# Performance work log

Hardware: AMD Instinct MI355X
Metric: run time of the kernel (lower is better)

Reference implementation:

```python
import jax, jax.numpy as jnp
import numpy as np

H = 8  # num_heads
C = 512  # embed_dims
L = 3  # num_layers
SCALE = (C // H) ** -0.5


def _ln(x, g, b, eps=1e-5):
    mu = jnp.mean(x, axis=-1, keepdims=True)
    var = jnp.mean((x - mu) ** 2, axis=-1, keepdims=True)
    return g * (x - mu) / jnp.sqrt(var + eps) + b


def setup_inputs() -> dict:
    key = jax.random.key(0)
    ks = jax.random.split(key, 12)
    B, Nq, Nk = 16, 64, 4096
    s = 0.02
    return dict(
        queries=jax.random.normal(ks[0], (B, Nq, C), jnp.float32),
        feat=jax.random.normal(ks[1], (B, Nk, C), jnp.float32),
        extra_token=jax.random.normal(ks[2], (B, 1, C), jnp.float32),
        Wq=jax.random.normal(ks[3], (L, C, C), jnp.float32) * s,
        bq=jnp.zeros((L, C), jnp.float32),
        Wk=jax.random.normal(ks[4], (L, C, C), jnp.float32) * s,
        bk=jnp.zeros((L, C), jnp.float32),
        Wv=jax.random.normal(ks[5], (L, C, C), jnp.float32) * s,
        bv=jnp.zeros((L, C), jnp.float32),
        Wo=jax.random.normal(ks[6], (L, C, C), jnp.float32) * s,
        bo=jnp.zeros((L, C), jnp.float32),
        W1=jax.random.normal(ks[7], (L, C, 4 * C), jnp.float32) * s,
        b1=jnp.zeros((L, 4 * C), jnp.float32),
        W2=jax.random.normal(ks[8], (L, 4 * C, C), jnp.float32) * s,
        b2=jnp.zeros((L, C), jnp.float32),
        g2=jnp.ones((L, C), jnp.float32),
        beta2=jnp.zeros((L, C), jnp.float32),
        g3=jnp.ones((L, C), jnp.float32),
        beta3=jnp.zeros((L, C), jnp.float32),
    )


def reference(queries, feat, extra_token, Wq, bq, Wk, bk, Wv, bv, Wo, bo,
              W1, b1, W2, b2, g2, beta2, g3, beta3):
    B, Nq, _ = queries.shape
    Nk = feat.shape[1]
    hd = C // H
    # extra gating token is NOT projected through q: raw reshape -> [B,H,1,hd]
    eq = extra_token.reshape(B, 1, H, hd).transpose(0, 2, 1, 3)
    x = queries
    outs, attns, affs = [], [], []
    for i in range(L):
        q = (x @ Wq[i] + bq[i]).reshape(B, Nq, H, hd).transpose(0, 2, 1, 3)
        k = (feat @ Wk[i] + bk[i]).reshape(B, Nk, H, hd).transpose(0, 2, 1, 3)
        v = (feat @ Wv[i] + bv[i]).reshape(B, Nk, H, hd).transpose(0, 2, 1, 3)
        attn = jnp.einsum('bhqd,bhkd->bhqk', q, k) * SCALE  # pre-softmax scores
        # affinity gate from extra token, averaged over heads -> [B,1,1,Nk]
        aff = jax.nn.sigmoid(jnp.mean(
            jnp.einsum('bhod,bhkd->bhok', eq, k) * SCALE, axis=1, keepdims=True))
        p = aff * jax.nn.softmax(attn, axis=-1)  # gated probabilities
        o = jnp.einsum('bhqk,bhkd->bqhd', p, v).reshape(B, Nq, C)
        o = o @ Wo[i] + bo[i]
        x = _ln(x + o, g2[i], beta2[i])
        ff = jax.nn.relu(x @ W1[i] + b1[i]) @ W2[i] + b2[i]
        x = _ln(x + ff, g3[i], beta3[i])
        outs.append(x)
        attns.append(attn.sum(axis=1) / H)  # head-averaged pre-softmax scores
        affs.append(aff)
    return (jnp.stack(outs), jnp.stack(attns), jnp.stack(affs))
```

## Files before the change

### kernel.cpp

```cpp
#include <hip/hip_runtime.h>


typedef unsigned short u16;
typedef __attribute__((ext_vector_type(8))) short short8;
typedef __attribute__((ext_vector_type(4))) short short4v;
typedef __attribute__((ext_vector_type(4))) float f32x4;

__device__ __forceinline__ float b2f(u16 u) {
    union { unsigned int i; float f; } v; v.i = ((unsigned int)u) << 16; return v.f;
}
__device__ __forceinline__ u16 f2b(float f) {
    unsigned int x = __float_as_uint(f);
    x += 0x7fffu + ((x >> 16) & 1u);
    return (u16)(x >> 16);
}

__device__ __forceinline__ float waveSum(float v) {
#pragma unroll
    for (int o = 32; o > 0; o >>= 1) v += __shfl_xor(v, o);
    return v;
}

__device__ __forceinline__ void gl_lds16(const void* g, void* l) {
    __builtin_amdgcn_global_load_lds(
        (__attribute__((address_space(1))) void*)g,
        (__attribute__((address_space(3))) void*)l, 16, 0, 0);
}

__global__ __launch_bounds__(256) void fattn_k(
    const u16* __restrict__ q16, const u16* __restrict__ K16,
    const u16* __restrict__ VT16, float* __restrict__ Op,
    float2* __restrict__ ml)
{
    __shared__ u16 Qs[64][64];
    __shared__ u16 Ks[128][64];
    __shared__ u16 Vs[64][128];
    __shared__ u16 Ps[64][128];
    const int t = threadIdx.x;
    const int lane = t & 63;
    const int w = t >> 6;
    const int bh = blockIdx.y;
    const int split = blockIdx.x;
    const int b = bh >> 3, h = bh & 7;
    const int kbase = split * 1024;
    const int rl = lane & 15, uq = lane >> 4;
    const int r0 = (lane >> 4) * 4;
    const int c0 = lane & 15;
    const int srow8 = lane >> 3, up8 = lane & 7;
    const int srow4 = lane >> 4, up16 = lane & 15;

#pragma unroll
    for (int rnd = 0; rnd < 2; ++rnd) {
        const int row = rnd * 32 + w * 8 + srow8;
        const int ul = up8 ^ (row & 7);
        gl_lds16(q16 + ((long)(b * 64 + row)) * 512 + h * 64 + ul * 8,
                 &Qs[rnd * 32 + w * 8][0]);
    }

    f32x4 O[4];
#pragma unroll
    for (int n = 0; n < 4; ++n) O[n] = (f32x4){0.f, 0.f, 0.f, 0.f};
    float m_run[4] = {-3.0e38f, -3.0e38f, -3.0e38f, -3.0e38f};
    float l_run[4] = {0.f, 0.f, 0.f, 0.f};

    const int R = w * 16 + rl;

    for (int tt = 0; tt < 8; ++tt) {
        __syncthreads();
#pragma unroll
        for (int rnd = 0; rnd < 4; ++rnd) {
            const int row = rnd * 32 + w * 8 + srow8;
            const int ul = up8 ^ (row & 7);
            gl_lds16(K16 + ((long)(b * 4096 + kbase + tt * 128 + row)) * 512
                         + h * 64 + ul * 8,
                     &Ks[rnd * 32 + w * 8][0]);
        }
#pragma unroll
        for (int rnd = 0; rnd < 4; ++rnd) {
            const int row = rnd * 16 + w * 4 + srow4;
            const int ul = up16 ^ (row & 15);
            gl_lds16(VT16 + (long)b * 2097152 + ((long)(h * 64 + row)) * 4096
                         + kbase + tt * 128 + ul * 8,
                     &Vs[rnd * 16 + w * 4][0]);
        }
        __syncthreads();

        f32x4 s[8];
        short8 af[2];
#pragma unroll
        for (int kc = 0; kc < 2; ++kc)
            af[kc] = *(const short8*)(&Qs[R][((kc * 4 + uq) ^ (R & 7)) * 8]);
#pragma unroll
        for (int j = 0; j < 8; ++j) {
            s[j] = (f32x4){0.f, 0.f, 0.f, 0.f};
            const int Rb = j * 16 + rl;
#pragma unroll
            for (int kc = 0; kc < 2; ++kc) {
                short8 bf = *(const short8*)(&Ks[Rb][((kc * 4 + uq) ^ (Rb & 7)) * 8]);
                s[j] = __builtin_amdgcn_mfma_f32_16x16x32_bf16(af[kc], bf, s[j], 0, 0, 0);
            }
        }
#pragma unroll
        for (int j = 0; j < 8; ++j)
#pragma unroll
            for (int r = 0; r < 4; ++r) s[j][r] *= 0.125f;

        float mv[4];
#pragma unroll
        for (int r = 0; r < 4; ++r) {
            float m = s[0][r];
#pragma unroll
            for (int j = 1; j < 8; ++j) m = fmaxf(m, s[j][r]);
#pragma unroll
            for (int mask = 1; mask < 16; mask <<= 1)
                m = fmaxf(m, __shfl_xor(m, mask));
            mv[r] = m;
        }
        float al[4], rs[4];
#pragma unroll
        for (int r = 0; r < 4; ++r) {
            const float mn = fmaxf(m_run[r], mv[r]);
            al[r] = __expf(m_run[r] - mn);
            m_run[r] = mn;
            rs[r] = 0.f;
        }
#pragma unroll
        for (int j = 0; j < 8; ++j)
#pragma unroll
            for (int r = 0; r < 4; ++r) {
                s[j][r] = __expf(s[j][r] - m_run[r]);
                rs[r] += s[j][r];
            }
#pragma unroll
        for (int r = 0; r < 4; ++r) {
#pragma unroll
            for (int mask = 1; mask < 16; mask <<= 1)
                rs[r] += __shfl_xor(rs[r], mask);
            l_run[r] = l_run[r] * al[r] + rs[r];
        }
#pragma unroll
        for (int n = 0; n < 4; ++n)
#pragma unroll
            for (int r = 0; r < 4; ++r) O[n][r] *= al[r];

#pragma unroll
        for (int j = 0; j < 8; ++j)
#pragma unroll
            for (int r = 0; r < 4; ++r) {
                const int row = w * 16 + r0 + r;
                const int col = j * 16 + c0;
                Ps[row][(((col >> 3) ^ (row & 15)) << 3) + (col & 7)] = f2b(s[j][r]);
            }
#pragma unroll
        for (int kc4 = 0; kc4 < 4; ++kc4) {
            const short8 afp = *(const short8*)(&Ps[R][(((kc4 * 4 + uq) ^ (R & 15)) << 3)]);
#pragma unroll
            for (int n = 0; n < 4; ++n) {
                const int Rv = n * 16 + rl;
                const short8 bfv = *(const short8*)(&Vs[Rv][(((kc4 * 4 + uq) ^ (Rv & 15)) << 3)]);
                O[n] = __builtin_amdgcn_mfma_f32_16x16x32_bf16(afp, bfv, O[n], 0, 0, 0);
            }
        }
    }

    const long obase = ((long)(split * 128 + bh)) * 64;
#pragma unroll
    for (int n = 0; n < 4; ++n)
#pragma unroll
        for (int r = 0; r < 4; ++r) {
            const int q = w * 16 + r0 + r;
            Op[(obase + q) * 64 + n * 16 + c0] = O[n][r];
        }
    if (c0 == 0) {
#pragma unroll
        for (int r = 0; r < 4; ++r) {
            const int q = w * 16 + r0 + r;
            ml[obase + q] = make_float2(m_run[r], l_run[r]);
        }
    }
}

__global__ __launch_bounds__(256) void fmerge_k(
    const float* __restrict__ Op, const float2* __restrict__ ml,
    u16* __restrict__ o16)
{
    const int i = blockIdx.x * 256 + threadIdx.x;
    const int d4 = i & 15;
    const int q  = (i >> 4) & 63;
    const int bh = i >> 10;
    const float2 m0 = ml[((long)(0 * 128 + bh)) * 64 + q];
    const float2 m1 = ml[((long)(1 * 128 + bh)) * 64 + q];
    const float2 m2 = ml[((long)(2 * 128 + bh)) * 64 + q];
    const float2 m3 = ml[((long)(3 * 128 + bh)) * 64 + q];
    const float m = fmaxf(fmaxf(m0.x, m1.x), fmaxf(m2.x, m3.x));
    const float e0 = __expf(m0.x - m), e1 = __expf(m1.x - m);
    const float e2 = __expf(m2.x - m), e3 = __expf(m3.x - m);
    const float inv = 1.f / (m0.y * e0 + m1.y * e1 + m2.y * e2 + m3.y * e3);
    const float4 v0 = *(const float4*)(Op + (((long)(0 * 128 + bh)) * 64 + q) * 64 + d4 * 4);
    const float4 v1 = *(const float4*)(Op + (((long)(1 * 128 + bh)) * 64 + q) * 64 + d4 * 4);
    const float4 v2 = *(const float4*)(Op + (((long)(2 * 128 + bh)) * 64 + q) * 64 + d4 * 4);
    const float4 v3 = *(const float4*)(Op + (((long)(3 * 128 + bh)) * 64 + q) * 64 + d4 * 4);
    float4 acc;
    acc.x = (v0.x * e0 + v1.x * e1 + v2.x * e2 + v3.x * e3) * inv;
    acc.y = (v0.y * e0 + v1.y * e1 + v2.y * e2 + v3.y * e3) * inv;
    acc.z = (v0.z * e0 + v1.z * e1 + v2.z * e2 + v3.z * e3) * inv;
    acc.w = (v0.w * e0 + v1.w * e1 + v2.w * e2 + v3.w * e3) * inv;
    const int b = bh >> 3, h = bh & 7;
    short4v r;
    r[0] = (short)f2b(acc.x); r[1] = (short)f2b(acc.y);
    r[2] = (short)f2b(acc.z); r[3] = (short)f2b(acc.w);
    *(short4v*)(o16 + (long)b * 32768 + q * 512 + h * 64 + d4 * 4) = r;
}

template<bool BIAS_ROW, bool HAS_BIAS, bool AFFC>
__global__ __launch_bounds__(512, 1) void gemm256x256_k(
    const u16* __restrict__ A, const u16* __restrict__ Bt,
    const float* __restrict__ bias, u16* __restrict__ Cout,
    int lda, int ldb, int ldc, long sA2, long sB2, long sC2,
    const float* __restrict__ affc)
{
    __shared__ u16 As[2][256][64];
    __shared__ u16 Bs[2][256][64];
    const int t = threadIdx.x;
    const int lane = t & 63;
    const int wave = t >> 6;

    const int gx = gridDim.x, gy = gridDim.y;
    const int nwg = gx * gy * gridDim.z;
    int id;
    {
        const int orig = blockIdx.x + blockIdx.y * gx + blockIdx.z * gx * gy;
        const int qq = nwg >> 3, rr = nwg & 7;
        const int xcd = orig & 7, sub = orig >> 3;
        id = (xcd < rr ? xcd * (qq + 1) : rr * (qq + 1) + (xcd - rr) * qq) + sub;
    }
    const int bx = id % gx;
    const int by = (id / gx) % gy;
    const int z  = id / (gx * gy);

    A  += (long)z * sA2;
    Bt += (long)z * sB2;
    const long cbase = (long)z * sC2;
    const int n0 = bx * 256;
    const int m0 = by * 256;
    const int wm = wave >> 2;
    const int wn = wave & 3;
    const int rl = lane & 15, uq = lane >> 4;
    const int srow = lane >> 3;
    const int up   = lane & 7;

    f32x4 acc[8][4];
#pragma unroll
    for (int i = 0; i < 8; ++i)
#pragma unroll
        for (int j = 0; j < 4; ++j) acc[i][j] = (f32x4){0.f, 0.f, 0.f, 0.f};

    auto stage = [&](int buf, int kt) {
        const int k0 = kt * 64;
#pragma unroll
        for (int r = 0; r < 4; ++r) {
            const int row = r * 64 + wave * 8 + srow;
            const int ul = up ^ (row & 7);
            gl_lds16(A + (long)(m0 + row) * lda + k0 + ul * 8,
                     &As[buf][r * 64 + wave * 8][0]);
        }
#pragma unroll
        for (int r = 0; r < 4; ++r) {
            const int row = r * 64 + wave * 8 + srow;
            const int ul = up ^ (row & 7);
            gl_lds16(Bt + (long)(n0 + row) * ldb + k0 + ul * 8,
                     &Bs[buf][r * 64 + wave * 8][0]);
        }
    };

    auto compute = [&](int buf) {
#pragma unroll
        for (int kc = 0; kc < 2; ++kc) {
            short8 af[8], bf[4];
#pragma unroll
            for (int i = 0; i < 8; ++i) {
                const int R = wm * 128 + i * 16 + rl;
                af[i] = *(const short8*)(&As[buf][R][((kc * 4 + uq) ^ (R & 7)) * 8]);
            }
#pragma unroll
            for (int j = 0; j < 4; ++j) {
                const int R = wn * 64 + j * 16 + rl;
                bf[j] = *(const short8*)(&Bs[buf][R][((kc * 4 + uq) ^ (R & 7)) * 8]);
            }
            __builtin_amdgcn_s_setprio(1);
#pragma unroll
            for (int i = 0; i < 8; ++i)
#pragma unroll
                for (int j = 0; j < 4; ++j)
                    acc[i][j] = __builtin_amdgcn_mfma_f32_16x16x32_bf16(
                        af[i], bf[j], acc[i][j], 0, 0, 0);
            __builtin_amdgcn_s_setprio(0);
        }
    };

    stage(0, 0);
    __syncthreads();
    int buf = 0;
#pragma unroll
    for (int kt = 0; kt < 8; ++kt) {
        if (kt + 1 < 8) stage(buf ^ 1, kt + 1);
        compute(buf);
        __syncthreads();
        buf ^= 1;
    }

    const int r0 = (lane >> 4) * 4;
    const int c0 = lane & 15;
#pragma unroll
    for (int i = 0; i < 8; ++i) {
#pragma unroll
        for (int j = 0; j < 4; ++j) {
#pragma unroll
            for (int r = 0; r < 4; ++r) {
                const int row = m0 + wm * 128 + i * 16 + r0 + r;
                const int col = n0 + wn * 64 + j * 16 + c0;
                float v = acc[i][j][r];
                if constexpr (HAS_BIAS) {
                    if constexpr (BIAS_ROW) v += bias[row]; else v += bias[col];
                }
                if constexpr (AFFC) v *= affc[(long)z * 4096 + col];
                Cout[cbase + (long)row * ldc + col] = f2b(v);
            }
        }
    }
}

template<int TM, int TN, bool OUT_BF16, bool RELU, bool BIAS_ROW, bool HAS_BIAS>
__global__ __launch_bounds__(256) void gemm_bt_k(
    const u16* __restrict__ A, const u16* __restrict__ Bt,
    const float* __restrict__ bias, void* __restrict__ Cout,
    int K, int lda, int ldb, int ldc,
    long sA1, long sB1, long sC1, float alpha)
{
    __shared__ u16 As[TM][64];
    __shared__ u16 Bs[TN][64];
    const int t = threadIdx.x;
    const int lane = t & 63;
    const int wave = t >> 6;
    const int z = blockIdx.z;
    A  += (long)z * sA1;
    Bt += (long)z * sB1;
    const long cbase = (long)z * sC1;
    const int n0 = blockIdx.x * TN;
    const int m0 = blockIdx.y * TM;
    constexpr int FM = TM / 32, FN = TN / 32;
    const int wr = wave >> 1, wc = wave & 1;
    const int rl = lane & 15, uq = lane >> 4;

    f32x4 acc[FM][FN];
#pragma unroll
    for (int i = 0; i < FM; ++i)
#pragma unroll
        for (int j = 0; j < FN; ++j) acc[i][j] = (f32x4){0.f, 0.f, 0.f, 0.f};

    const int srow = lane >> 3;
    const int up   = lane & 7;

    for (int k0 = 0; k0 < K; k0 += 64) {
        __syncthreads();
#pragma unroll
        for (int r = 0; r < TM / 32; ++r) {
            const int br = (wave * (TM / 32) + r) * 8;
            const int row = br + srow;
            const int ul = up ^ (row & 7);
            gl_lds16(A + (long)(m0 + row) * lda + k0 + ul * 8, &As[br][0]);
        }
#pragma unroll
        for (int r = 0; r < TN / 32; ++r) {
            const int br = (wave * (TN / 32) + r) * 8;
            const int row = br + srow;
            const int ul = up ^ (row & 7);
            gl_lds16(Bt + (long)(n0 + row) * ldb + k0 + ul * 8, &Bs[br][0]);
        }
        __syncthreads();

#pragma unroll
        for (int kc = 0; kc < 2; ++kc) {
            short8 af[FM], bf[FN];
#pragma unroll
            for (int i = 0; i < FM; ++i) {
                const int R = wr * (TM / 2) + i * 16 + rl;
                af[i] = *(const short8*)(&As[R][((kc * 4 + uq) ^ (R & 7)) * 8]);
            }
#pragma unroll
            for (int j = 0; j < FN; ++j) {
                const int R = wc * (TN / 2) + j * 16 + rl;
                bf[j] = *(const short8*)(&Bs[R][((kc * 4 + uq) ^ (R & 7)) * 8]);
            }
#pragma unroll
            for (int i = 0; i < FM; ++i)
#pragma unroll
                for (int j = 0; j < FN; ++j)
                    acc[i][j] = __builtin_amdgcn_mfma_f32_16x16x32_bf16(
                        af[i], bf[j], acc[i][j], 0, 0, 0);
        }
    }

    const int r0 = (lane >> 4) * 4;
    const int c0 = lane & 15;
#pragma unroll
    for (int i = 0; i < FM; ++i) {
#pragma unroll
        for (int j = 0; j < FN; ++j) {
#pragma unroll
            for (int r = 0; r < 4; ++r) {
                const int row = m0 + wr * (TM / 2) + i * 16 + r0 + r;
                const int col = n0 + wc * (TN / 2) + j * 16 + c0;
                float v = acc[i][j][r] * alpha;
                if constexpr (HAS_BIAS) {
                    if constexpr (BIAS_ROW) v += bias[row]; else v += bias[col];
                }
                if constexpr (RELU) v = fmaxf(v, 0.f);
                const long idx = cbase + (long)row * ldc + col;
                if constexpr (OUT_BF16) ((u16*)Cout)[idx] = f2b(v);
                else                    ((float*)Cout)[idx] = v;
            }
        }
    }
}

__global__ __launch_bounds__(256) void ffred_k(
    const float* __restrict__ part, const float* __restrict__ bias,
    float* __restrict__ out)
{
    const int i = (blockIdx.x * 256 + threadIdx.x) * 4;
    const int c = i & 511;
    float4 s = *(const float4*)(part + i);
#pragma unroll
    for (int sp = 1; sp < 4; ++sp) {
        const float4 v = *(const float4*)(part + (long)sp * 524288 + i);
        s.x += v.x; s.y += v.y; s.z += v.z; s.w += v.w;
    }
    s.x += bias[c]; s.y += bias[c + 1]; s.z += bias[c + 2]; s.w += bias[c + 3];
    *(float4*)(out + i) = s;
}

__global__ __launch_bounds__(256) void umat_k(
    const float* __restrict__ Wk, const float* __restrict__ extra,
    float* __restrict__ u)
{
    __shared__ float ex[16][512];
    const int l = blockIdx.x;
    const int t = threadIdx.x;
    for (int i = t; i < 16 * 512 / 4; i += 256)
        ((float4*)&ex[0][0])[i] = ((const float4*)extra)[i];
    __syncthreads();
    const int lane = t & 63, wave = t >> 6;
    const int row = blockIdx.y * 4 + wave;
    const float* wrow = Wk + ((size_t)l * 512 + row) * 512 + lane * 8;
    float w[8];
#pragma unroll
    for (int j = 0; j < 8; ++j) w[j] = wrow[j];
    float s[16];
#pragma unroll
    for (int b = 0; b < 16; ++b) {
        float x = 0.f;
#pragma unroll
        for (int j = 0; j < 8; ++j) x += w[j] * ex[b][lane * 8 + j];
        s[b] = waveSum(x);
    }
    if (lane < 16) u[((size_t)l * 16 + lane) * 512 + row] = s[lane];
}

__global__ __launch_bounds__(256) void cbk_k(
    const float* __restrict__ bk, const float* __restrict__ extra,
    float* __restrict__ cb)
{
    const int gw = blockIdx.x * 4 + (threadIdx.x >> 6);
    const int lane = threadIdx.x & 63;
    const int l = gw >> 4, b = gw & 15;
    float s = 0.f;
#pragma unroll
    for (int j = 0; j < 8; ++j)
        s += extra[b * 512 + lane * 8 + j] * bk[l * 512 + lane * 8 + j];
    s = waveSum(s);
    if (lane == 0) cb[gw] = s;
}

__global__ __launch_bounds__(256) void cvt16_aff_k(
    const float* __restrict__ feat, u16* __restrict__ dst,
    const float* __restrict__ u, const float* __restrict__ cb,
    float* __restrict__ affb, float* __restrict__ affs_out)
{
    const int t = blockIdx.x * 256 + threadIdx.x;
    const long i = (long)t * 8;
    const int lane = threadIdx.x & 63;
    const int r = t >> 6;
    const int b = r >> 12;
    const float4 a0 = *(const float4*)(feat + i);
    const float4 a1 = *(const float4*)(feat + i + 4);
    short8 o;
    o[0] = (short)f2b(a0.x); o[1] = (short)f2b(a0.y);
    o[2] = (short)f2b(a0.z); o[3] = (short)f2b(a0.w);
    o[4] = (short)f2b(a1.x); o[5] = (short)f2b(a1.y);
    o[6] = (short)f2b(a1.z); o[7] = (short)f2b(a1.w);
    *(short8*)(dst + i) = o;
    const float f[8] = {a0.x, a0.y, a0.z, a0.w, a1.x, a1.y, a1.z, a1.w};
#pragma unroll
    for (int l = 0; l < 3; ++l) {
        const float* ur = u + ((size_t)l * 16 + b) * 512 + lane * 8;
        float s = 0.f;
#pragma unroll
        for (int j = 0; j < 8; ++j) s += f[j] * ur[j];
        s = waveSum(s);
        if (lane == 0) {
            const float av = 1.f / (1.f + __expf(-0.015625f * (s + cb[l * 16 + b])));
            affb[l * 65536 + r] = av;
            affs_out[l * 65536 + r] = av;
        }
    }
}

template<bool WRITE_OUT>
__global__ __launch_bounds__(256) void ln_k(
    float* __restrict__ x, const float* __restrict__ add,
    const float* __restrict__ g, const float* __restrict__ be,
    u16* __restrict__ x16, float* __restrict__ outp)
{
    const int r = blockIdx.x, t = threadIdx.x;
    const int w = t >> 6, lane = t & 63;
    __shared__ float red[4];
    float* xr = x + (long)r * 512;
    const float* ar = add + (long)r * 512;
    const float v0 = xr[2 * t]     + ar[2 * t];
    const float v1 = xr[2 * t + 1] + ar[2 * t + 1];
    float s = waveSum(v0 + v1);
    if (lane == 0) red[w] = s;
    __syncthreads();
    s = red[0] + red[1] + red[2] + red[3];
    const float mu = s * (1.f / 512.f);
    const float d0 = v0 - mu, d1 = v1 - mu;
    __syncthreads();
    float vs = waveSum(d0 * d0 + d1 * d1);
    if (lane == 0) red[w] = vs;
    __syncthreads();
    vs = red[0] + red[1] + red[2] + red[3];
    const float rs = rsqrtf(vs * (1.f / 512.f) + 1e-5f);
    const float o0 = g[2 * t]     * d0 * rs + be[2 * t];
    const float o1 = g[2 * t + 1] * d1 * rs + be[2 * t + 1];
    xr[2 * t] = o0; xr[2 * t + 1] = o1;
    x16[(long)r * 512 + 2 * t]     = f2b(o0);
    x16[(long)r * 512 + 2 * t + 1] = f2b(o1);
    if constexpr (WRITE_OUT) {
        outp[(long)r * 512 + 2 * t]     = o0;
        outp[(long)r * 512 + 2 * t + 1] = o1;
    }
}

__global__ __launch_bounds__(256) void initx_k(
    const float* __restrict__ src, float* __restrict__ x, u16* __restrict__ x16)
{
    const long i = ((long)blockIdx.x * 256 + threadIdx.x) * 8;
    const float4 a = *(const float4*)(src + i);
    const float4 b = *(const float4*)(src + i + 4);
    *(float4*)(x + i) = a;
    *(float4*)(x + i + 4) = b;
    short8 r;
    r[0] = (short)f2b(a.x); r[1] = (short)f2b(a.y); r[2] = (short)f2b(a.z); r[3] = (short)f2b(a.w);
    r[4] = (short)f2b(b.x); r[5] = (short)f2b(b.y); r[6] = (short)f2b(b.z); r[7] = (short)f2b(b.w);
    *(short8*)(x16 + i) = r;
}

__global__ __launch_bounds__(256) void transpose_w_k(
    const float* __restrict__ W, u16* __restrict__ WT, int K, int N)
{
    __shared__ float tile[32][33];
    const int z = blockIdx.z;
    W  += (size_t)z * K * N;
    WT += (size_t)z * K * N;
    const int n0 = blockIdx.x * 32, k0 = blockIdx.y * 32;
    const int tx = threadIdx.x & 31, ty = threadIdx.x >> 5;
#pragma unroll
    for (int j = 0; j < 32; j += 8)
        tile[ty + j][tx] = W[(size_t)(k0 + ty + j) * N + n0 + tx];
    __syncthreads();
#pragma unroll
    for (int j = 0; j < 32; j += 8)
        WT[(size_t)(n0 + ty + j) * K + k0 + tx] = f2b(tile[tx][ty + j]);
}

extern "C" void kernel_launch(void* const* d_in, const int* in_sizes, int n_in,
                              void* d_out, int out_size, void* d_ws, size_t ws_size,
                              hipStream_t stream)
{
    (void)in_sizes; (void)n_in; (void)out_size; (void)ws_size;
    const float* queries = (const float*)d_in[0];
    const float* feat    = (const float*)d_in[1];
    const float* extra   = (const float*)d_in[2];
    const float* Wq = (const float*)d_in[3];  const float* bq = (const float*)d_in[4];
    const float* Wk = (const float*)d_in[5];  const float* bk = (const float*)d_in[6];
    const float* Wv = (const float*)d_in[7];  const float* bv = (const float*)d_in[8];
    const float* Wo = (const float*)d_in[9];  const float* bo = (const float*)d_in[10];
    const float* W1 = (const float*)d_in[11]; const float* b1 = (const float*)d_in[12];
    const float* W2 = (const float*)d_in[13]; const float* b2 = (const float*)d_in[14];
    const float* g2 = (const float*)d_in[15]; const float* be2 = (const float*)d_in[16];
    const float* g3 = (const float*)d_in[17]; const float* be3 = (const float*)d_in[18];

    char* wsb = (char*)d_ws;
    size_t off = 0;
    auto alloc = [&](size_t bytes) -> char* {
        char* p = wsb + off; off += (bytes + 255) & ~(size_t)255; return p;
    };
    u16*  feat16 = (u16*)alloc(33554432ull * 2);
    u16*  WqT = (u16*)alloc(786432ull * 2);
    u16*  WkT = (u16*)alloc(786432ull * 2);
    u16*  WvT = (u16*)alloc(786432ull * 2);
    u16*  WoT = (u16*)alloc(786432ull * 2);
    u16*  W1T = (u16*)alloc(3145728ull * 2);
    u16*  W2T = (u16*)alloc(3145728ull * 2);
    u16*  K16 = (u16*)alloc(33554432ull * 2);
    u16*  VT16 = (u16*)alloc(33554432ull * 2);
    u16*  q16 = (u16*)alloc(524288ull * 2);
    float* Op  = (float*)alloc(4194304ull * 4);
    float2* ml = (float2*)alloc(32768ull * 8);
    float* affb  = (float*)alloc(196608ull * 4);
    u16*  o16 = (u16*)alloc(524288ull * 2);
    float* oproj = (float*)alloc(524288ull * 4);
    float* xb    = (float*)alloc(524288ull * 4);
    u16*  x16 = (u16*)alloc(524288ull * 2);
    u16*  h116 = (u16*)alloc(2097152ull * 2);
    float* ffb   = (float*)alloc(524288ull * 4);
    float* uvec  = (float*)alloc(24576ull * 4);
    float* cb    = (float*)alloc(48ull * 4);
    float* part2 = (float*)VT16;

    float* out_f = (float*)d_out;
    float* outs_base  = out_f;
    float* attns_base = out_f + 1572864;
    float* affs_base  = out_f + 14155776;

    umat_k<<<dim3(3, 128), 256, 0, stream>>>(Wk, extra, uvec);
    cbk_k<<<12, 256, 0, stream>>>(bk, extra, cb);
    cvt16_aff_k<<<16384, 256, 0, stream>>>(feat, feat16, uvec, cb, affb, affs_base);
    initx_k<<<256, 256, 0, stream>>>(queries, xb, x16);
    transpose_w_k<<<dim3(16, 16, 3), 256, 0, stream>>>(Wq, WqT, 512, 512);
    transpose_w_k<<<dim3(16, 16, 3), 256, 0, stream>>>(Wk, WkT, 512, 512);
    transpose_w_k<<<dim3(16, 16, 3), 256, 0, stream>>>(Wv, WvT, 512, 512);
    transpose_w_k<<<dim3(16, 16, 3), 256, 0, stream>>>(Wo, WoT, 512, 512);
    transpose_w_k<<<dim3(64, 16, 3), 256, 0, stream>>>(W1, W1T, 512, 2048);
    transpose_w_k<<<dim3(16, 64, 3), 256, 0, stream>>>(W2, W2T, 2048, 512);

    for (int i = 0; i < 3; ++i) {
        gemm256x256_k<false, true, false><<<dim3(2, 256, 1), 512, 0, stream>>>(
            feat16, WkT + i * 262144, bk + i * 512, K16,
            512, 512, 512, 0, 0, 0, nullptr);
        gemm256x256_k<true, true, true><<<dim3(16, 2, 16), 512, 0, stream>>>(
            WvT + i * 262144, feat16, bv + i * 512, VT16,
            512, 512, 4096, 0, 2097152, 2097152, affb + i * 65536);
        gemm_bt_k<64, 64, true, false, false, true>
            <<<dim3(8, 16, 1), 256, 0, stream>>>(
            x16, WqT + i * 262144, bq + i * 512, q16,
            512, 512, 512, 512, 0, 0, 0, 1.f);
        gemm_bt_k<64, 128, false, false, false, false>
            <<<dim3(32, 1, 16), 256, 0, stream>>>(
            q16, K16, nullptr, attns_base + (size_t)i * 4194304,
            512, 512, 512, 4096, 32768, 2097152, 262144, 0.015625f);
        fattn_k<<<dim3(4, 128), 256, 0, stream>>>(q16, K16, VT16, Op, ml);
        fmerge_k<<<512, 256, 0, stream>>>(Op, ml, o16);
        gemm_bt_k<64, 64, false, false, false, true>
            <<<dim3(8, 16, 1), 256, 0, stream>>>(
            o16, WoT + i * 262144, bo + i * 512, oproj,
            512, 512, 512, 512, 0, 0, 0, 1.f);
        ln_k<false><<<1024, 256, 0, stream>>>(xb, oproj, g2 + i * 512, be2 + i * 512, x16, nullptr);
        gemm_bt_k<64, 128, true, true, false, true>
            <<<dim3(16, 16, 1), 256, 0, stream>>>(
            x16, W1T + (size_t)i * 1048576, b1 + i * 2048, h116,
            512, 512, 512, 2048, 0, 0, 0, 1.f);
        gemm_bt_k<64, 64, false, false, false, false>
            <<<dim3(8, 16, 4), 256, 0, stream>>>(
            h116, W2T + (size_t)i * 1048576, nullptr, part2,
            512, 2048, 2048, 512, 512, 512, 524288, 1.f);
        ffred_k<<<512, 256, 0, stream>>>(part2, b2 + i * 512, ffb);
        ln_k<true><<<1024, 256, 0, stream>>>(xb, ffb, g3 + i * 512, be3 + i * 512, x16,
                                             outs_base + (size_t)i * 524288);
    }
}
```

Measured before the change: 670.1 us.

## Interleave global-to-LDS staging with MFMA phases in 256x256 GEMM

Result: slower. 688.7 us (+2.8%).

```diff
diff --git a/kernel.cpp b/kernel.cpp
--- a/kernel.cpp
+++ b/kernel.cpp
@@ -25,6 +25,136 @@
     __builtin_amdgcn_global_load_lds(
         (__attribute__((address_space(1))) void*)g,
         (__attribute__((address_space(3))) void*)l, 16, 0, 0);
+}
+
+template<bool BIAS_ROW, bool HAS_BIAS, bool AFFC>
+__global__ __launch_bounds__(512, 1) void gemm256x256_k(
+    const u16* __restrict__ A, const u16* __restrict__ Bt,
+    const float* __restrict__ bias, u16* __restrict__ Cout,
+    int lda, int ldb, int ldc, long sA2, long sB2, long sC2,
+    const float* __restrict__ affc)
+{
+    __shared__ u16 As[2][256][64];
+    __shared__ u16 Bs[2][256][64];
+    const int t = threadIdx.x;
+    const int lane = t & 63;
+    const int wave = t >> 6;
+
+    const int gx = gridDim.x, gy = gridDim.y;
+    const int nwg = gx * gy * gridDim.z;
+    int id;
+    {
+        const int orig = blockIdx.x + blockIdx.y * gx + blockIdx.z * gx * gy;
+        const int qq = nwg >> 3, rr = nwg & 7;
+        const int xcd = orig & 7, sub = orig >> 3;
+        id = (xcd < rr ? xcd * (qq + 1) : rr * (qq + 1) + (xcd - rr) * qq) + sub;
+    }
+    const int bx = id % gx;
+    const int by = (id / gx) % gy;
+    const int z  = id / (gx * gy);
+
+    A  += (long)z * sA2;
+    Bt += (long)z * sB2;
+    const long cbase = (long)z * sC2;
+    const int n0 = bx * 256;
+    const int m0 = by * 256;
+    const int wm = wave >> 2;
+    const int wn = wave & 3;
+    const int rl = lane & 15, uq = lane >> 4;
+    const int srow = lane >> 3;
+    const int up   = lane & 7;
+
+    f32x4 acc[8][4];
+#pragma unroll
+    for (int i = 0; i < 8; ++i)
+#pragma unroll
+        for (int j = 0; j < 4; ++j) acc[i][j] = (f32x4){0.f, 0.f, 0.f, 0.f};
+
+    auto stage_round = [&](int buf, int kt, int rnd) {
+        const int k0 = kt * 64;
+        if (rnd < 4) {
+            const int row = rnd * 64 + wave * 8 + srow;
+            const int ul = up ^ (row & 7);
+            gl_lds16(A + (long)(m0 + row) * lda + k0 + ul * 8,
+                     &As[buf][rnd * 64 + wave * 8][0]);
+        } else {
+            const int r = rnd - 4;
+            const int row = r * 64 + wave * 8 + srow;
+            const int ul = up ^ (row & 7);
+            gl_lds16(Bt + (long)(n0 + row) * ldb + k0 + ul * 8,
+                     &Bs[buf][r * 64 + wave * 8][0]);
+        }
+    };
+
+#pragma unroll
+    for (int rnd = 0; rnd < 8; ++rnd) stage_round(0, 0, rnd);
+    __syncthreads();
+
+    int buf = 0;
+    for (int kt = 0; kt < 8; ++kt) {
+        const int nbuf = buf ^ 1;
+        short8 bf[2][4];
+#pragma unroll
+        for (int p = 0; p < 4; ++p) {
+            if (kt < 7) {
+                stage_round(nbuf, kt + 1, p * 2);
+                stage_round(nbuf, kt + 1, p * 2 + 1);
+            }
+            if (p == 0) {
+#pragma unroll
+                for (int kc = 0; kc < 2; ++kc)
+#pragma unroll
+                    for (int j = 0; j < 4; ++j) {
+                        const int Rb = wn * 64 + j * 16 + rl;
+                        bf[kc][j] = *(const short8*)(
+                            &Bs[buf][Rb][((kc * 4 + uq) ^ (Rb & 7)) * 8]);
+                    }
+            }
+            short8 af[2][2];
+#pragma unroll
+            for (int kc = 0; kc < 2; ++kc)
+#pragma unroll
+                for (int i2 = 0; i2 < 2; ++i2) {
+                    const int Ra = wm * 128 + (p * 2 + i2) * 16 + rl;
+                    af[kc][i2] = *(const short8*)(
+                        &As[buf][Ra][((kc * 4 + uq) ^ (Ra & 7)) * 8]);
+                }
+            __builtin_amdgcn_s_barrier();
+            __builtin_amdgcn_s_setprio(1);
+#pragma unroll
+            for (int kc = 0; kc < 2; ++kc)
+#pragma unroll
+                for (int i2 = 0; i2 < 2; ++i2)
+#pragma unroll
+                    for (int j = 0; j < 4; ++j)
+                        acc[p * 2 + i2][j] = __builtin_amdgcn_mfma_f32_16x16x32_bf16(
+                            af[kc][i2], bf[kc][j], acc[p * 2 + i2][j], 0, 0, 0);
+            __builtin_amdgcn_s_setprio(0);
+            if (p < 3) __builtin_amdgcn_s_barrier();
+        }
+        __syncthreads();
+        buf = nbuf;
+    }
+
+    const int r0 = (lane >> 4) * 4;
+    const int c0 = lane & 15;
+#pragma unroll
+    for (int i = 0; i < 8; ++i) {
+#pragma unroll
+        for (int j = 0; j < 4; ++j) {
+#pragma unroll
+            for (int r = 0; r < 4; ++r) {
+                const int row = m0 + wm * 128 + i * 16 + r0 + r;
+                const int col = n0 + wn * 64 + j * 16 + c0;
+                float v = acc[i][j][r];
+                if constexpr (HAS_BIAS) {
+                    if constexpr (BIAS_ROW) v += bias[row]; else v += bias[col];
+                }
+                if constexpr (AFFC) v *= affc[(long)z * 4096 + col];
+                Cout[cbase + (long)row * ldc + col] = f2b(v);
+            }
+        }
+    }
 }
 
 __global__ __launch_bounds__(256) void fattn_k(
@@ -210,124 +340,6 @@
     r[0] = (short)f2b(acc.x); r[1] = (short)f2b(acc.y);
     r[2] = (short)f2b(acc.z); r[3] = (short)f2b(acc.w);
     *(short4v*)(o16 + (long)b * 32768 + q * 512 + h * 64 + d4 * 4) = r;
-}
-
-template<bool BIAS_ROW, bool HAS_BIAS, bool AFFC>
-__global__ __launch_bounds__(512, 1) void gemm256x256_k(
-    const u16* __restrict__ A, const u16* __restrict__ Bt,
-    const float* __restrict__ bias, u16* __restrict__ Cout,
-    int lda, int ldb, int ldc, long sA2, long sB2, long sC2,
-    const float* __restrict__ affc)
-{
-    __shared__ u16 As[2][256][64];
-    __shared__ u16 Bs[2][256][64];
-    const int t = threadIdx.x;
-    const int lane = t & 63;
-    const int wave = t >> 6;
-
-    const int gx = gridDim.x, gy = gridDim.y;
-    const int nwg = gx * gy * gridDim.z;
-    int id;
-    {
-        const int orig = blockIdx.x + blockIdx.y * gx + blockIdx.z * gx * gy;
-        const int qq = nwg >> 3, rr = nwg & 7;
-        const int xcd = orig & 7, sub = orig >> 3;
-        id = (xcd < rr ? xcd * (qq + 1) : rr * (qq + 1) + (xcd - rr) * qq) + sub;
-    }
-    const int bx = id % gx;
-    const int by = (id / gx) % gy;
-    const int z  = id / (gx * gy);
-
-    A  += (long)z * sA2;
-    Bt += (long)z * sB2;
-    const long cbase = (long)z * sC2;
-    const int n0 = bx * 256;
-    const int m0 = by * 256;
-    const int wm = wave >> 2;
-    const int wn = wave & 3;
-    const int rl = lane & 15, uq = lane >> 4;
-    const int srow = lane >> 3;
-    const int up   = lane & 7;
-
-    f32x4 acc[8][4];
-#pragma unroll
-    for (int i = 0; i < 8; ++i)
-#pragma unroll
-        for (int j = 0; j < 4; ++j) acc[i][j] = (f32x4){0.f, 0.f, 0.f, 0.f};
-
-    auto stage = [&](int buf, int kt) {
-        const int k0 = kt * 64;
-#pragma unroll
-        for (int r = 0; r < 4; ++r) {
-            const int row = r * 64 + wave * 8 + srow;
-            const int ul = up ^ (row & 7);
-            gl_lds16(A + (long)(m0 + row) * lda + k0 + ul * 8,
-                     &As[buf][r * 64 + wave * 8][0]);
-        }
-#pragma unroll
-        for (int r = 0; r < 4; ++r) {
-            const int row = r * 64 + wave * 8 + srow;
-            const int ul = up ^ (row & 7);
-            gl_lds16(Bt + (long)(n0 + row) * ldb + k0 + ul * 8,
-                     &Bs[buf][r * 64 + wave * 8][0]);
-        }
-    };
-
-    auto compute = [&](int buf) {
-#pragma unroll
-        for (int kc = 0; kc < 2; ++kc) {
-            short8 af[8], bf[4];
-#pragma unroll
-            for (int i = 0; i < 8; ++i) {
-                const int R = wm * 128 + i * 16 + rl;
-                af[i] = *(const short8*)(&As[buf][R][((kc * 4 + uq) ^ (R & 7)) * 8]);
-            }
-#pragma unroll
-            for (int j = 0; j < 4; ++j) {
-                const int R = wn * 64 + j * 16 + rl;
-                bf[j] = *(const short8*)(&Bs[buf][R][((kc * 4 + uq) ^ (R & 7)) * 8]);
-            }
-            __builtin_amdgcn_s_setprio(1);
-#pragma unroll
-            for (int i = 0; i < 8; ++i)
-#pragma unroll
-                for (int j = 0; j < 4; ++j)
-                    acc[i][j] = __builtin_amdgcn_mfma_f32_16x16x32_bf16(
-                        af[i], bf[j], acc[i][j], 0, 0, 0);
-            __builtin_amdgcn_s_setprio(0);
-        }
-    };
-
-    stage(0, 0);
-    __syncthreads();
-    int buf = 0;
-#pragma unroll
-    for (int kt = 0; kt < 8; ++kt) {
-        if (kt + 1 < 8) stage(buf ^ 1, kt + 1);
-        compute(buf);
-        __syncthreads();
-        buf ^= 1;
-    }
-
-    const int r0 = (lane >> 4) * 4;
-    const int c0 = lane & 15;
-#pragma unroll
-    for (int i = 0; i < 8; ++i) {
-#pragma unroll
-        for (int j = 0; j < 4; ++j) {
-#pragma unroll
-            for (int r = 0; r < 4; ++r) {
-                const int row = m0 + wm * 128 + i * 16 + r0 + r;
-                const int col = n0 + wn * 64 + j * 16 + c0;
-                float v = acc[i][j][r];
-                if constexpr (HAS_BIAS) {
-                    if constexpr (BIAS_ROW) v += bias[row]; else v += bias[col];
-                }
-                if constexpr (AFFC) v *= affc[(long)z * 4096 + col];
-                Cout[cbase + (long)row * ldc + col] = f2b(v);
-            }
-        }
-    }
 }
 
 template<int TM, int TN, bool OUT_BF16, bool RELU, bool BIAS_ROW, bool HAS_BIAS>
```

## Pipeline 256x256 GEMM with four-slot half-K stages and split barriers

Applied to the files above, without the earlier changes.

New measurement: 660.3 us. Within noise of the previous version (-1.5%).

```diff
diff --git a/kernel.cpp b/kernel.cpp
--- a/kernel.cpp
+++ b/kernel.cpp
@@ -25,6 +25,174 @@
     __builtin_amdgcn_global_load_lds(
         (__attribute__((address_space(1))) void*)g,
         (__attribute__((address_space(3))) void*)l, 16, 0, 0);
+}
+
+template<bool BIAS_ROW, bool HAS_BIAS, bool AFFC>
+__global__ __launch_bounds__(512, 1) void gemm256v2_k(
+    const u16* __restrict__ A, const u16* __restrict__ Bt,
+    const float* __restrict__ bias, u16* __restrict__ Cout,
+    int lda, int ldb, int ldc, long sA2, long sB2, long sC2,
+    const float* __restrict__ affc)
+{
+    __shared__ u16 Ah[4][256][32];
+    __shared__ u16 Bh[4][256][32];
+    const int tid = threadIdx.x;
+    const int lane = tid & 63;
+    const int wave = tid >> 6;
+
+    const int gx = gridDim.x, gy = gridDim.y;
+    const int nwg = gx * gy * gridDim.z;
+    int id;
+    {
+        const int orig = blockIdx.x + blockIdx.y * gx + blockIdx.z * gx * gy;
+        const int qq = nwg >> 3, rr = nwg & 7;
+        const int xcd = orig & 7, sub = orig >> 3;
+        id = (xcd < rr ? xcd * (qq + 1) : rr * (qq + 1) + (xcd - rr) * qq) + sub;
+    }
+    const int bx = id % gx;
+    const int by = (id / gx) % gy;
+    const int z  = id / (gx * gy);
+
+    A  += (long)z * sA2;
+    Bt += (long)z * sB2;
+    const long cbase = (long)z * sC2;
+    const int n0 = bx * 256;
+    const int m0 = by * 256;
+    const int wm = wave >> 2;
+    const int wn = wave & 3;
+    const int rl = lane & 15;
+    const int uq = lane >> 4;
+    const int srow = lane >> 2;
+    const int up   = lane & 3;
+
+    f32x4 acc[8][4];
+#pragma unroll
+    for (int i = 0; i < 8; ++i)
+#pragma unroll
+        for (int j = 0; j < 4; ++j) acc[i][j] = (f32x4){0.f, 0.f, 0.f, 0.f};
+
+    auto stage_round = [&](int h, int r) {
+        const int slot = h & 3;
+        const int k0 = h * 32;
+        if (r < 2) {
+            const int row = r * 128 + wave * 16 + srow;
+            const int ul = up ^ ((row >> 2) & 3);
+            gl_lds16(A + (long)(m0 + row) * lda + k0 + ul * 8,
+                     &Ah[slot][r * 128 + wave * 16][0]);
+        } else {
+            const int row = (r - 2) * 128 + wave * 16 + srow;
+            const int ul = up ^ ((row >> 2) & 3);
+            gl_lds16(Bt + (long)(n0 + row) * ldb + k0 + ul * 8,
+                     &Bh[slot][(r - 2) * 128 + wave * 16][0]);
+        }
+    };
+
+#pragma unroll
+    for (int h = 0; h < 3; ++h)
+#pragma unroll
+        for (int r = 0; r < 4; ++r) stage_round(h, r);
+    asm volatile("s_waitcnt vmcnt(8)\n\ts_barrier" ::: "memory");
+
+#pragma unroll
+    for (int t = 0; t < 8; ++t) {
+        const int s0 = (2 * t) & 3, s1 = (2 * t + 1) & 3;
+        const int hA = 2 * t + 3, hB = 2 * t + 4;
+        short8 bf[4], af[4];
+
+        if (hA < 16) { stage_round(hA, 0); stage_round(hA, 1); }
+#pragma unroll
+        for (int j = 0; j < 4; ++j) {
+            const int R = wn * 64 + j * 16 + rl;
+            bf[j] = *(const short8*)(&Bh[s0][R][(uq ^ ((R >> 2) & 3)) * 8]);
+        }
+#pragma unroll
+        for (int i = 0; i < 4; ++i) {
+            const int R = wm * 128 + i * 16 + rl;
+            af[i] = *(const short8*)(&Ah[s0][R][(uq ^ ((R >> 2) & 3)) * 8]);
+        }
+        __builtin_amdgcn_s_setprio(1);
+#pragma unroll
+        for (int i = 0; i < 4; ++i)
+#pragma unroll
+            for (int j = 0; j < 4; ++j)
+                acc[i][j] = __builtin_amdgcn_mfma_f32_16x16x32_bf16(
+                    af[i], bf[j], acc[i][j], 0, 0, 0);
+        __builtin_amdgcn_s_setprio(0);
+
+        if (hA < 16) { stage_round(hA, 2); stage_round(hA, 3); }
+#pragma unroll
+        for (int i = 0; i < 4; ++i) {
+            const int R = wm * 128 + (4 + i) * 16 + rl;
+            af[i] = *(const short8*)(&Ah[s0][R][(uq ^ ((R >> 2) & 3)) * 8]);
+        }
+        __builtin_amdgcn_s_setprio(1);
+#pragma unroll
+        for (int i = 0; i < 4; ++i)
+#pragma unroll
+            for (int j = 0; j < 4; ++j)
+                acc[4 + i][j] = __builtin_amdgcn_mfma_f32_16x16x32_bf16(
+                    af[i], bf[j], acc[4 + i][j], 0, 0, 0);
+        __builtin_amdgcn_s_setprio(0);
+        if (t < 7) asm volatile("s_waitcnt vmcnt(8)\n\ts_barrier" ::: "memory");
+        else       asm volatile("s_waitcnt vmcnt(0)\n\ts_barrier" ::: "memory");
+
+        if (hB < 16) { stage_round(hB, 0); stage_round(hB, 1); }
+#pragma unroll
+        for (int j = 0; j < 4; ++j) {
+            const int R = wn * 64 + j * 16 + rl;
+            bf[j] = *(const short8*)(&Bh[s1][R][(uq ^ ((R >> 2) & 3)) * 8]);
+        }
+#pragma unroll
+        for (int i = 0; i < 4; ++i) {
+            const int R = wm * 128 + i * 16 + rl;
+            af[i] = *(const short8*)(&Ah[s1][R][(uq ^ ((R >> 2) & 3)) * 8]);
+        }
+        __builtin_amdgcn_s_setprio(1);
+#pragma unroll
+        for (int i = 0; i < 4; ++i)
+#pragma unroll
+            for (int j = 0; j < 4; ++j)
+                acc[i][j] = __builtin_amdgcn_mfma_f32_16x16x32_bf16(
+                    af[i], bf[j], acc[i][j], 0, 0, 0);
+        __builtin_amdgcn_s_setprio(0);
+
+        if (hB < 16) { stage_round(hB, 2); stage_round(hB, 3); }
+#pragma unroll
+        for (int i = 0; i < 4; ++i) {
+            const int R = wm * 128 + (4 + i) * 16 + rl;
+            af[i] = *(const short8*)(&Ah[s1][R][(uq ^ ((R >> 2) & 3)) * 8]);
+        }
+        __builtin_amdgcn_s_setprio(1);
+#pragma unroll
+        for (int i = 0; i < 4; ++i)
+#pragma unroll
+            for (int j = 0; j < 4; ++j)
+                acc[4 + i][j] = __builtin_amdgcn_mfma_f32_16x16x32_bf16(
+                    af[i], bf[j], acc[4 + i][j], 0, 0, 0);
+        __builtin_amdgcn_s_setprio(0);
+        if (t < 6)       asm volatile("s_waitcnt vmcnt(8)\n\ts_barrier" ::: "memory");
+        else if (t == 6) asm volatile("s_waitcnt vmcnt(4)\n\ts_barrier" ::: "memory");
+    }
+
+    const int r0 = (lane >> 4) * 4;
+    const int c0 = lane & 15;
+#pragma unroll
+    for (int i = 0; i < 8; ++i) {
+#pragma unroll
+        for (int j = 0; j < 4; ++j) {
+#pragma unroll
+            for (int r = 0; r < 4; ++r) {
+                const int row = m0 + wm * 128 + i * 16 + r0 + r;
+                const int col = n0 + wn * 64 + j * 16 + c0;
+                float v = acc[i][j][r];
+                if constexpr (HAS_BIAS) {
+                    if constexpr (BIAS_ROW) v += bias[row]; else v += bias[col];
+                }
+                if constexpr (AFFC) v *= affc[(long)z * 4096 + col];
+                Cout[cbase + (long)row * ldc + col] = f2b(v);
+            }
+        }
+    }
 }
 
 __global__ __launch_bounds__(256) void fattn_k(
@@ -210,124 +378,6 @@
     r[0] = (short)f2b(acc.x); r[1] = (short)f2b(acc.y);
     r[2] = (short)f2b(acc.z); r[3] = (short)f2b(acc.w);
     *(short4v*)(o16 + (long)b * 32768 + q * 512 + h * 64 + d4 * 4) = r;
-}
-
-template<bool BIAS_ROW, bool HAS_BIAS, bool AFFC>
-__global__ __launch_bounds__(512, 1) void gemm256x256_k(
-    const u16* __restrict__ A, const u16* __restrict__ Bt,
-    const float* __restrict__ bias, u16* __restrict__ Cout,
-    int lda, int ldb, int ldc, long sA2, long sB2, long sC2,
-    const float* __restrict__ affc)
-{
-    __shared__ u16 As[2][256][64];
-    __shared__ u16 Bs[2][256][64];
-    const int t = threadIdx.x;
-    const int lane = t & 63;
-    const int wave = t >> 6;
-
-    const int gx = gridDim.x, gy = gridDim.y;
-    const int nwg = gx * gy * gridDim.z;
-    int id;
-    {
-        const int orig = blockIdx.x + blockIdx.y * gx + blockIdx.z * gx * gy;
-        const int qq = nwg >> 3, rr = nwg & 7;
-        const int xcd = orig & 7, sub = orig >> 3;
-        id = (xcd < rr ? xcd * (qq + 1) : rr * (qq + 1) + (xcd - rr) * qq) + sub;
-    }
-    const int bx = id % gx;
-    const int by = (id / gx) % gy;
-    const int z  = id / (gx * gy);
-
-    A  += (long)z * sA2;
-    Bt += (long)z * sB2;
-    const long cbase = (long)z * sC2;
-    const int n0 = bx * 256;
-    const int m0 = by * 256;
-    const int wm = wave >> 2;
-    const int wn = wave & 3;
-    const int rl = lane & 15, uq = lane >> 4;
-    const int srow = lane >> 3;
-    const int up   = lane & 7;
-
-    f32x4 acc[8][4];
-#pragma unroll
-    for (int i = 0; i < 8; ++i)
-#pragma unroll
-        for (int j = 0; j < 4; ++j) acc[i][j] = (f32x4){0.f, 0.f, 0.f, 0.f};
-
-    auto stage = [&](int buf, int kt) {
-        const int k0 = kt * 64;
-#pragma unroll
-        for (int r = 0; r < 4; ++r) {
-            const int row = r * 64 + wave * 8 + srow;
-            const int ul = up ^ (row & 7);
-            gl_lds16(A + (long)(m0 + row) * lda + k0 + ul * 8,
-                     &As[buf][r * 64 + wave * 8][0]);
-        }
-#pragma unroll
-        for (int r = 0; r < 4; ++r) {
-            const int row = r * 64 + wave * 8 + srow;
-            const int ul = up ^ (row & 7);
-            gl_lds16(Bt + (long)(n0 + row) * ldb + k0 + ul * 8,
-                     &Bs[buf][r * 64 + wave * 8][0]);
-        }
-    };
-
-    auto compute = [&](int buf) {
-#pragma unroll
-        for (int kc = 0; kc < 2; ++kc) {
-            short8 af[8], bf[4];
-#pragma unroll
-            for (int i = 0; i < 8; ++i) {
-                const int R = wm * 128 + i * 16 + rl;
-                af[i] = *(const short8*)(&As[buf][R][((kc * 4 + uq) ^ (R & 7)) * 8]);
-            }
-#pragma unroll
-            for (int j = 0; j < 4; ++j) {
-                const int R = wn * 64 + j * 16 + rl;
-                bf[j] = *(const short8*)(&Bs[buf][R][((kc * 4 + uq) ^ (R & 7)) * 8]);
-            }
-            __builtin_amdgcn_s_setprio(1);
-#pragma unroll
-            for (int i = 0; i < 8; ++i)
-#pragma unroll
-                for (int j = 0; j < 4; ++j)
-                    acc[i][j] = __builtin_amdgcn_mfma_f32_16x16x32_bf16(
-                        af[i], bf[j], acc[i][j], 0, 0, 0);
-            __builtin_amdgcn_s_setprio(0);
-        }
-    };
-
-    stage(0, 0);
-    __syncthreads();
-    int buf = 0;
-#pragma unroll
-    for (int kt = 0; kt < 8; ++kt) {
-        if (kt + 1 < 8) stage(buf ^ 1, kt + 1);
-        compute(buf);
-        __syncthreads();
-        buf ^= 1;
-    }
-
-    const int r0 = (lane >> 4) * 4;
-    const int c0 = lane & 15;
-#pragma unroll
-    for (int i = 0; i < 8; ++i) {
-#pragma unroll
-        for (int j = 0; j < 4; ++j) {
-#pragma unroll
-            for (int r = 0; r < 4; ++r) {
-                const int row = m0 + wm * 128 + i * 16 + r0 + r;
-                const int col = n0 + wn * 64 + j * 16 + c0;
-                float v = acc[i][j][r];
-                if constexpr (HAS_BIAS) {
-                    if constexpr (BIAS_ROW) v += bias[row]; else v += bias[col];
-                }
-                if constexpr (AFFC) v *= affc[(long)z * 4096 + col];
-                Cout[cbase + (long)row * ldc + col] = f2b(v);
-            }
-        }
-    }
 }
 
 template<int TM, int TN, bool OUT_BF16, bool RELU, bool BIAS_ROW, bool HAS_BIAS>
@@ -646,10 +696,10 @@
     transpose_w_k<<<dim3(16, 64, 3), 256, 0, stream>>>(W2, W2T, 2048, 512);
 
     for (int i = 0; i < 3; ++i) {
-        gemm256x256_k<false, true, false><<<dim3(2, 256, 1), 512, 0, stream>>>(
+        gemm256v2_k<false, true, false><<<dim3(2, 256, 1), 512, 0, stream>>>(
             feat16, WkT + i * 262144, bk + i * 512, K16,
             512, 512, 512, 0, 0, 0, nullptr);
-        gemm256x256_k<true, true, true><<<dim3(16, 2, 16), 512, 0, stream>>>(
+        gemm256v2_k<true, true, true><<<dim3(16, 2, 16), 512, 0, stream>>>(
             WvT + i * 262144, feat16, bv + i * 512, VT16,
             512, 512, 4096, 0, 2097152, 2097152, affb + i * 65536);
         gemm_bt_k<64, 64, true, false, false, true>
```
